# Kernel optimization log

Measured on AMD Instinct MI355X. Metric: run time of the kernel, lower is better.

## Reference

```python
import jax, jax.numpy as jnp
import numpy as np

B, S, HID = 1, 4096, 2048
NH, NKV, D = 16, 4, 128           # num_heads, num_kv_heads, head_dim
QPG = NH // NKV                   # q heads per kv group
GROUP = (QPG + 2) * D             # fused per-group width: Q..Q K V
TOTAL = NKV * GROUP


def setup_inputs() -> dict:
    key = jax.random.key(0)
    k0, k1, k2 = jax.random.split(key, 3)
    x = jax.random.normal(k0, (B, S, HID), dtype=jnp.float32)
    weight_qkv = jax.random.normal(k1, (TOTAL, HID), dtype=jnp.float32) * 0.02
    weight_proj = jax.random.normal(k2, (HID, NH * D), dtype=jnp.float32) * 0.02
    return {"x": x, "weight_qkv": weight_qkv, "weight_proj": weight_proj}


def reference(x, weight_qkv, weight_proj):
    b, s, _ = x.shape
    # fused QKV projection, grouped layout: [b, s, NKV, (QPG+2)*D]
    qkv = jnp.einsum('bsh,ph->bsp', x, weight_qkv).reshape(b, s, NKV, GROUP)
    q = qkv[..., : QPG * D].reshape(b, s, NKV, QPG, D)      # [b,s,g,q,d]
    k = qkv[..., QPG * D:(QPG + 1) * D]                      # [b,s,g,d]
    v = qkv[..., (QPG + 1) * D:]                             # [b,s,g,d]

    scale = 1.0 / jnp.sqrt(jnp.float32(D))
    # GQA causal attention (ring attention at cp_size=1 == full causal attn)
    scores = jnp.einsum('bsgqd,btgd->bgqst', q, k) * scale   # [b,g,q,s,s]
    causal = jnp.tril(jnp.ones((s, s), dtype=bool))
    scores = jnp.where(causal, scores, jnp.finfo(scores.dtype).min)
    attn = jax.nn.softmax(scores, axis=-1)
    out = jnp.einsum('bgqst,btgd->bsgqd', attn, v)           # [b,s,g,q,d]
    out = out.reshape(b, s, NH * D)
    return jnp.einsum('bse,he->bsh', out, weight_proj)       # [b,s,HID]
```

## Files before the change

### kernel.cpp

```cpp
#include <hip/hip_runtime.h>
#include <hip/hip_bf16.h>
#include <stdint.h>

typedef __attribute__((ext_vector_type(8))) short short8;
typedef __attribute__((ext_vector_type(4))) float f32x4;

#define S_LEN   4096
#define HID_DIM 2048
#define NHEAD   16
#define NKV     4
#define DHEAD   128
#define QPG     4
#define GROUP   768
#define TOTAL   3072

#define EXP2F(x) __builtin_amdgcn_exp2f(x)

__device__ __forceinline__ ushort f2bf(float f) {
    union { float f; uint32_t u; } c; c.f = f;
    uint32_t u = c.u;
    u += 0x7fff + ((u >> 16) & 1);
    return (ushort)(u >> 16);
}
__device__ __forceinline__ float bf2f(ushort u) {
    union { uint32_t u; float f; } c; c.u = ((uint32_t)u) << 16;
    return c.f;
}

__device__ __forceinline__ void gld_lds16(const void* g, void* l) {
    __builtin_amdgcn_global_load_lds(
        (const __attribute__((address_space(1))) void*)g,
        (__attribute__((address_space(3))) void*)l, 16, 0, 0);
}

__global__ __launch_bounds__(256)
void cvt_f32_bf16(const float* __restrict__ src, ushort* __restrict__ dst,
                  int n4, int mode)
{
    int i = blockIdx.x * blockDim.x + threadIdx.x;
    int stride = gridDim.x * blockDim.x;
    for (; i < n4; i += stride) {
        float sc = 1.0f;
        if (mode == 1) {
            int row = i >> 9;
            sc = ((row % GROUP) < QPG * DHEAD) ? 0.12751744157413583f : 1.0f;
        }
        float4 v = ((const float4*)src)[i];
        ushort4 o;
        o.x = f2bf(v.x * sc); o.y = f2bf(v.y * sc);
        o.z = f2bf(v.z * sc); o.w = f2bf(v.w * sc);
        ((ushort4*)dst)[i] = o;
    }
}

__device__ __forceinline__ void store_c(ushort* C, size_t idx, float v) { C[idx] = f2bf(v); }
__device__ __forceinline__ void store_c(float*  C, size_t idx, float v) { C[idx] = v; }

template <typename OutT, int NJ, bool WRITE_VT>
__global__ __launch_bounds__(256, 2)
void gemm_bt(const ushort* __restrict__ A, const ushort* __restrict__ B,
             OutT* __restrict__ C, ushort* __restrict__ VT,
             int M, int N, int K)
{
    __shared__ alignas(16) ushort Asl[128 * 32];
    __shared__ alignas(16) ushort Bsl[NJ * 32 * 32];

    const int tid  = threadIdx.x;
    const int wave = tid >> 6;
    const int lane = tid & 63;
    const int quad = lane >> 4;
    const int l15  = lane & 15;
    const int wr   = wave >> 1;
    const int wc   = wave & 1;
    const int m0   = blockIdx.y * 128;
    const int n0   = blockIdx.x * (32 * NJ);

    f32x4 acc[4][NJ];
#pragma unroll
    for (int i = 0; i < 4; i++)
#pragma unroll
        for (int j = 0; j < NJ; j++) acc[i][j] = (f32x4)0.0f;

    for (int kb = 0; kb < K; kb += 32) {
        __syncthreads();
#pragma unroll
        for (int k = 0; k < 2 + NJ / 2; k++) {
            int idx = k * 256 + tid;
            if (idx < 512) {
                const ushort* g = A + (size_t)(m0 + (idx >> 2)) * K + kb + (idx & 3) * 8;
                gld_lds16(g, (char*)Asl + (size_t)(k * 256 + wave * 64) * 16);
            } else {
                int j = idx - 512;
                const ushort* g = B + (size_t)(n0 + (j >> 2)) * K + kb + (j & 3) * 8;
                gld_lds16(g, (char*)Bsl + (size_t)((k - 2) * 256 + wave * 64) * 16);
            }
        }
        __syncthreads();

        short8 af[4], bf[NJ];
#pragma unroll
        for (int i = 0; i < 4; i++)
            af[i] = *(const short8*)(&Asl[(wr * 64 + i * 16 + l15) * 32 + quad * 8]);
#pragma unroll
        for (int j = 0; j < NJ; j++)
            bf[j] = *(const short8*)(&Bsl[(wc * 16 * NJ + j * 16 + l15) * 32 + quad * 8]);
#pragma unroll
        for (int i = 0; i < 4; i++)
#pragma unroll
            for (int j = 0; j < NJ; j++)
                acc[i][j] = __builtin_amdgcn_mfma_f32_16x16x32_bf16(
                    af[i], bf[j], acc[i][j], 0, 0, 0);
    }

#pragma unroll
    for (int j = 0; j < NJ; j++) {
        const int colb = n0 + wc * 16 * NJ + j * 16;
        const int cgrp = colb % GROUP;
        if (WRITE_VT && cgrp >= (QPG + 1) * DHEAD) {
            const int g = colb / GROUP;
            const int d = cgrp - (QPG + 1) * DHEAD + l15;
#pragma unroll
            for (int i = 0; i < 4; i++) {
                int row0 = m0 + wr * 64 + i * 16 + quad * 4;
                ushort4 pk;
                pk.x = f2bf(acc[i][j][0]); pk.y = f2bf(acc[i][j][1]);
                pk.z = f2bf(acc[i][j][2]); pk.w = f2bf(acc[i][j][3]);
                *(ushort4*)(VT + (size_t)(g * 128 + d) * S_LEN + row0) = pk;
            }
        } else {
#pragma unroll
            for (int i = 0; i < 4; i++)
#pragma unroll
                for (int r = 0; r < 4; r++) {
                    int row = m0 + wr * 64 + i * 16 + quad * 4 + r;
                    store_c(C, (size_t)row * N + colb + l15, acc[i][j][r]);
                }
        }
    }
}

__global__ __launch_bounds__(256, 2)
void flash_attn(const ushort* __restrict__ qkv, const ushort* __restrict__ VT,
                ushort* __restrict__ out, ushort* __restrict__ o_part,
                float* __restrict__ l_part)
{
    const int b    = blockIdx.x;
    const int head = b >> 5;
    const int pair = (b >> 1) & 15;
    const int half = b & 1;
    const int g    = head >> 2;
    const int qh   = head & 3;
    const int p_h  = 31 - pair;
    const int H    = 2 * p_h + 2;
    const int hslot = (head * 16 + pair) * 2 + half;

    const int tid  = threadIdx.x;
    const int wave = tid >> 6;
    const int lane = tid & 63;
    const int quad = lane >> 4;
    const int l15  = lane & 15;

    __shared__ alignas(16) ushort Kl[64][136];
    __shared__ alignas(16) ushort Vt[128][72];
    __shared__ alignas(16) ushort Pl[4][32][66];

    int seg_p[2], seg_t0[2], seg_t1[2], seg_part[2];
    int nseg;
    if (half == 0) {
        nseg = 1;
        seg_p[0] = p_h;  seg_t0[0] = 0;  seg_t1[0] = 33;           seg_part[0] = 1;
    } else {
        nseg = 2;
        seg_p[0] = p_h;  seg_t0[0] = 33; seg_t1[0] = H;            seg_part[0] = 1;
        seg_p[1] = pair; seg_t0[1] = 0;  seg_t1[1] = 2 * pair + 2; seg_part[1] = 0;
    }

    const int koff = g * GROUP + QPG * DHEAD;

    for (int s = 0; s < nseg; s++) {
        const int p  = seg_p[s];
        const int t0 = seg_t0[s];
        const int t1 = seg_t1[s];
        const int q0 = p * 128;
        const int base = q0 + wave * 32;

        short8 qf[2][4];
#pragma unroll
        for (int nq = 0; nq < 2; nq++) {
            int row = base + nq * 16 + l15;
            const ushort* qp = qkv + (size_t)row * TOTAL + g * GROUP + qh * DHEAD + quad * 8;
#pragma unroll
            for (int ks = 0; ks < 4; ks++)
                qf[nq][ks] = *(const short8*)(qp + ks * 32);
        }

        f32x4 o[2][8];
#pragma unroll
        for (int oq = 0; oq < 2; oq++)
#pragma unroll
            for (int df = 0; df < 8; df++) o[oq][df] = (f32x4)0.0f;
        float l_vec[2] = {0.0f, 0.0f};

        float4 kpre[4], vpre[4];
#pragma unroll
        for (int r = 0; r < 4; r++) {
            int c = tid + r * 256;
            int kr = c >> 4, kc = c & 15;
            kpre[r] = *(const float4*)(qkv + (size_t)(t0 * 64 + kr) * TOTAL + koff + kc * 8);
            int vd = c >> 3, vc = c & 7;
            vpre[r] = *(const float4*)(VT + (size_t)(g * 128 + vd) * S_LEN + t0 * 64 + vc * 8);
        }

        for (int t = t0; t < t1; t++) {
            __syncthreads();
#pragma unroll
            for (int r = 0; r < 4; r++) {
                int c = tid + r * 256;
                int kr = c >> 4, kc = c & 15;
                *(float4*)(&Kl[kr][kc * 8]) = kpre[r];
                int vd = c >> 3, vc = c & 7;
                *(float4*)(&Vt[vd][vc * 8]) = vpre[r];
            }
            __syncthreads();

            if (t + 1 < t1) {
                const int j1 = (t + 1) * 64;
#pragma unroll
                for (int r = 0; r < 4; r++) {
                    int c = tid + r * 256;
                    int kr = c >> 4, kc = c & 15;
                    kpre[r] = *(const float4*)(qkv + (size_t)(j1 + kr) * TOTAL + koff + kc * 8);
                    int vd = c >> 3, vc = c & 7;
                    vpre[r] = *(const float4*)(VT + (size_t)(g * 128 + vd) * S_LEN + j1 + vc * 8);
                }
            }

            const int j0 = t * 64;
            f32x4 sacc[4][2];
#pragma unroll
            for (int mk = 0; mk < 4; mk++)
#pragma unroll
                for (int nq = 0; nq < 2; nq++) sacc[mk][nq] = (f32x4)0.0f;
#pragma unroll
            for (int mk = 0; mk < 4; mk++)
#pragma unroll
                for (int ks = 0; ks < 4; ks++) {
                    short8 kf = *(const short8*)(&Kl[mk * 16 + l15][ks * 32 + quad * 8]);
#pragma unroll
                    for (int nq = 0; nq < 2; nq++)
                        sacc[mk][nq] = __builtin_amdgcn_mfma_f32_16x16x32_bf16(
                            kf, qf[nq][ks], sacc[mk][nq], 0, 0, 0);
                }

#pragma unroll
            for (int nq = 0; nq < 2; nq++) {
                const int qg = base + nq * 16 + l15;
#pragma unroll
                for (int mk = 0; mk < 4; mk++) {
                    float e0, e1, e2, e3;
                    if (j0 + mk * 16 + 15 > base + nq * 16) {
                        int kv = j0 + mk * 16 + quad * 4;
                        e0 = (kv + 0 > qg) ? 0.0f : EXP2F(sacc[mk][nq][0]);
                        e1 = (kv + 1 > qg) ? 0.0f : EXP2F(sacc[mk][nq][1]);
                        e2 = (kv + 2 > qg) ? 0.0f : EXP2F(sacc[mk][nq][2]);
                        e3 = (kv + 3 > qg) ? 0.0f : EXP2F(sacc[mk][nq][3]);
                    } else {
                        e0 = EXP2F(sacc[mk][nq][0]);
                        e1 = EXP2F(sacc[mk][nq][1]);
                        e2 = EXP2F(sacc[mk][nq][2]);
                        e3 = EXP2F(sacc[mk][nq][3]);
                    }
                    l_vec[nq] += (e0 + e1) + (e2 + e3);
                    ushort4 pk;
                    pk.x = f2bf(e0); pk.y = f2bf(e1);
                    pk.z = f2bf(e2); pk.w = f2bf(e3);
                    *(ushort4*)(&Pl[wave][nq * 16 + l15][mk * 16 + quad * 4]) = pk;
                }
            }

#pragma unroll
            for (int ks = 0; ks < 2; ks++) {
                short8 pf[2];
#pragma unroll
                for (int oq = 0; oq < 2; oq++)
                    pf[oq] = *(const short8*)(&Pl[wave][oq * 16 + l15][ks * 32 + quad * 8]);
#pragma unroll
                for (int df = 0; df < 8; df++) {
                    short8 vf = *(const short8*)(&Vt[df * 16 + l15][ks * 32 + quad * 8]);
#pragma unroll
                    for (int oq = 0; oq < 2; oq++)
                        o[oq][df] = __builtin_amdgcn_mfma_f32_16x16x32_bf16(
                            pf[oq], vf, o[oq][df], 0, 0, 0);
                }
            }
        }

        float l_full[2];
#pragma unroll
        for (int nq = 0; nq < 2; nq++) {
            float l = l_vec[nq];
            l += __shfl_xor(l, 16);
            l += __shfl_xor(l, 32);
            l_full[nq] = l;
        }

        if (seg_part[s]) {
            ushort* po = o_part + (size_t)hslot * 16384;
#pragma unroll
            for (int nq = 0; nq < 2; nq++)
                if (quad == 0)
                    l_part[hslot * 128 + wave * 32 + nq * 16 + l15] = l_full[nq];
#pragma unroll
            for (int oq = 0; oq < 2; oq++)
#pragma unroll
                for (int r = 0; r < 4; r++) {
                    int row_l = wave * 32 + oq * 16 + quad * 4 + r;
#pragma unroll
                    for (int df = 0; df < 8; df++)
                        po[row_l * 128 + df * 16 + l15] = f2bf(o[oq][df][r]);
                }
        } else {
#pragma unroll
            for (int oq = 0; oq < 2; oq++)
#pragma unroll
                for (int r = 0; r < 4; r++) {
                    float lq = __shfl(l_full[oq], quad * 4 + r);
                    float inv = 1.0f / lq;
                    int row = base + oq * 16 + quad * 4 + r;
#pragma unroll
                    for (int df = 0; df < 8; df++) {
                        float v = o[oq][df][r] * inv;
                        out[(size_t)row * (NHEAD * DHEAD) + head * DHEAD
                            + df * 16 + l15] = f2bf(v);
                    }
                }
        }
    }
}

__global__ __launch_bounds__(256)
void fixup_norm(const ushort* __restrict__ o_part, const float* __restrict__ l_part,
                ushort* __restrict__ attn)
{
    const int slot = blockIdx.x;
    const int head = slot >> 4;
    const int pair = slot & 15;
    const int q0   = (31 - pair) * 128;
    const int t    = threadIdx.x;
    const ushort* p0 = o_part + (size_t)(slot * 2) * 16384;
    const ushort* p1 = p0 + 16384;
#pragma unroll 4
    for (int i = 0; i < 64; i++) {
        int idx = i * 256 + t;
        int row = idx >> 7, d = idx & 127;
        float l = l_part[(slot * 2) * 128 + row] + l_part[(slot * 2 + 1) * 128 + row];
        float v = (bf2f(p0[idx]) + bf2f(p1[idx])) / l;
        attn[(size_t)(q0 + row) * HID_DIM + head * DHEAD + d] = f2bf(v);
    }
}

extern "C" void kernel_launch(void* const* d_in, const int* in_sizes, int n_in,
                              void* d_out, int out_size, void* d_ws, size_t ws_size,
                              hipStream_t stream)
{
    const float* x     = (const float*)d_in[0];
    const float* wqkv  = (const float*)d_in[1];
    const float* wproj = (const float*)d_in[2];
    float* outp = (float*)d_out;

    const size_t n_x     = (size_t)S_LEN * HID_DIM;
    const size_t n_wqkv  = (size_t)TOTAL * HID_DIM;
    const size_t n_wproj = (size_t)HID_DIM * HID_DIM;
    const size_t n_qkv   = (size_t)S_LEN * TOTAL;
    const size_t n_attn  = (size_t)S_LEN * HID_DIM;

    ushort* xb     = (ushort*)d_ws;
    ushort* wqkvb  = xb + n_x;
    ushort* qkv    = wqkvb + n_wqkv;
    ushort* attn   = qkv + n_qkv;
    ushort* vt     = attn + n_attn;
    ushort* o_part = xb;
    float*  l_part = (float*)wqkvb;
    ushort* wprojb = wqkvb;

    cvt_f32_bf16<<<2048, 256, 0, stream>>>(x, xb, (int)(n_x / 4), 0);
    cvt_f32_bf16<<<2048, 256, 0, stream>>>(wqkv, wqkvb, (int)(n_wqkv / 4), 1);

    gemm_bt<ushort, 6, true><<<dim3(TOTAL / 192, S_LEN / 128), 256, 0, stream>>>(
        xb, wqkvb, qkv, vt, S_LEN, TOTAL, HID_DIM);

    flash_attn<<<512, 256, 0, stream>>>(qkv, vt, attn, o_part, l_part);
    fixup_norm<<<256, 256, 0, stream>>>(o_part, l_part, attn);

    cvt_f32_bf16<<<2048, 256, 0, stream>>>(wproj, wprojb, (int)(n_wproj / 4), 0);
    gemm_bt<float, 4, false><<<dim3(HID_DIM / 128, S_LEN / 128), 256, 0, stream>>>(
        attn, wprojb, outp, nullptr, S_LEN, HID_DIM, HID_DIM);
}
```

Baseline: 425.3 us.

## Split causal attention work into three equal chunks per query-block pair

Reworks the flash-attention work split from two halves per paired query block to three equal 22-tile chunks over the combined high and low causal rows. This gives 768 blocks with an occupancy hint of 3, which should balance load across CUs and reduce the tail. The fixup kernel now merges up to three partial results per row block and uses ushort4 vectorised loads and stores. The cost is more partial writes and more fixup traffic, plus extra register pressure from the raised launch bound.

```diff
diff --git a/kernel.cpp b/kernel.cpp
--- a/kernel.cpp
+++ b/kernel.cpp
@@ -139,20 +139,21 @@
     }
 }
 
-__global__ __launch_bounds__(256, 2)
+__global__ __launch_bounds__(256, 3)
 void flash_attn(const ushort* __restrict__ qkv, const ushort* __restrict__ VT,
                 ushort* __restrict__ out, ushort* __restrict__ o_part,
                 float* __restrict__ l_part)
 {
     const int b    = blockIdx.x;
-    const int head = b >> 5;
-    const int pair = (b >> 1) & 15;
-    const int half = b & 1;
+    const int head = b / 48;
+    const int rem  = b % 48;
+    const int p    = rem / 3;
+    const int k    = rem % 3;
+    const int pairid = head * 16 + p;
     const int g    = head >> 2;
     const int qh   = head & 3;
-    const int p_h  = 31 - pair;
-    const int H    = 2 * p_h + 2;
-    const int hslot = (head * 16 + pair) * 2 + half;
+    const int T_h  = 64 - 2 * p;
+    const int T_l  = 2 * p + 2;
 
     const int tid  = threadIdx.x;
     const int wave = tid >> 6;
@@ -164,24 +165,33 @@
     __shared__ alignas(16) ushort Vt[128][72];
     __shared__ alignas(16) ushort Pl[4][32][66];
 
-    int seg_p[2], seg_t0[2], seg_t1[2], seg_part[2];
-    int nseg;
-    if (half == 0) {
-        nseg = 1;
-        seg_p[0] = p_h;  seg_t0[0] = 0;  seg_t1[0] = 33;           seg_part[0] = 1;
-    } else {
-        nseg = 2;
-        seg_p[0] = p_h;  seg_t0[0] = 33; seg_t1[0] = H;            seg_part[0] = 1;
-        seg_p[1] = pair; seg_t0[1] = 0;  seg_t1[1] = 2 * pair + 2; seg_part[1] = 0;
+    int sq0[2], st0[2], st1[2], sslot[2], spart[2];
+    int nseg = 0;
+    {
+        const int g0 = 22 * k, g1 = g0 + 22;
+        int a1 = (g1 < T_h) ? g1 : T_h;
+        if (g0 < a1) {
+            sq0[nseg] = 128 * (31 - p); st0[nseg] = g0; st1[nseg] = a1;
+            spart[nseg] = 1; sslot[nseg] = pairid * 3 + k; nseg++;
+        }
+        int b0 = (g0 > T_h) ? g0 : T_h;
+        if (b0 < g1) {
+            int t0l = b0 - T_h, t1l = g1 - T_h;
+            int full = (t0l == 0 && t1l == T_l);
+            sq0[nseg] = 128 * p; st0[nseg] = t0l; st1[nseg] = t1l;
+            spart[nseg] = !full;
+            sslot[nseg] = (k == 1) ? (pairid * 3 + 2)
+                                   : (768 + head * 5 + (p - 11));
+            nseg++;
+        }
     }
 
     const int koff = g * GROUP + QPG * DHEAD;
 
     for (int s = 0; s < nseg; s++) {
-        const int p  = seg_p[s];
-        const int t0 = seg_t0[s];
-        const int t1 = seg_t1[s];
-        const int q0 = p * 128;
+        const int t0 = st0[s];
+        const int t1 = st1[s];
+        const int q0 = sq0[s];
         const int base = q0 + wave * 32;
 
         short8 qf[2][4];
@@ -304,12 +314,13 @@
             l_full[nq] = l;
         }
 
-        if (seg_part[s]) {
-            ushort* po = o_part + (size_t)hslot * 16384;
+        if (spart[s]) {
+            const int slot = sslot[s];
+            ushort* po = o_part + (size_t)slot * 16384;
 #pragma unroll
             for (int nq = 0; nq < 2; nq++)
                 if (quad == 0)
-                    l_part[hslot * 128 + wave * 32 + nq * 16 + l15] = l_full[nq];
+                    l_part[slot * 128 + wave * 32 + nq * 16 + l15] = l_full[nq];
 #pragma unroll
             for (int oq = 0; oq < 2; oq++)
 #pragma unroll
@@ -342,20 +353,40 @@
 void fixup_norm(const ushort* __restrict__ o_part, const float* __restrict__ l_part,
                 ushort* __restrict__ attn)
 {
-    const int slot = blockIdx.x;
-    const int head = slot >> 4;
-    const int pair = slot & 15;
-    const int q0   = (31 - pair) * 128;
-    const int t    = threadIdx.x;
-    const ushort* p0 = o_part + (size_t)(slot * 2) * 16384;
-    const ushort* p1 = p0 + 16384;
-#pragma unroll 4
-    for (int i = 0; i < 64; i++) {
-        int idx = i * 256 + t;
-        int row = idx >> 7, d = idx & 127;
-        float l = l_part[(slot * 2) * 128 + row] + l_part[(slot * 2 + 1) * 128 + row];
-        float v = (bf2f(p0[idx]) + bf2f(p1[idx])) / l;
-        attn[(size_t)(q0 + row) * HID_DIM + head * DHEAD + d] = f2bf(v);
+    const int bid = blockIdx.x;
+    int head, p, q0, ns, sl[3];
+    if (bid < 256) {
+        head = bid >> 4; p = bid & 15;
+        q0 = 128 * (31 - p);
+        ns = (p < 10) ? 3 : 2;
+        int bs = (head * 16 + p) * 3;
+        sl[0] = bs; sl[1] = bs + 1; sl[2] = bs + 2;
+    } else {
+        int idx = bid - 256;
+        head = idx / 5; p = 11 + idx % 5;
+        q0 = 128 * p;
+        ns = 2;
+        sl[0] = (head * 16 + p) * 3 + 2;
+        sl[1] = 768 + head * 5 + (p - 11);
+        sl[2] = 0;
+    }
+    const int t = threadIdx.x;
+#pragma unroll 2
+    for (int i = 0; i < 16; i++) {
+        int e4  = i * 256 + t;
+        int row = e4 >> 5;
+        int d4  = (e4 & 31) * 4;
+        float l = 0.0f, v0 = 0.0f, v1 = 0.0f, v2 = 0.0f, v3 = 0.0f;
+        for (int j = 0; j < ns; j++) {
+            l += l_part[sl[j] * 128 + row];
+            ushort4 u = *(const ushort4*)(o_part + (size_t)sl[j] * 16384 + row * 128 + d4);
+            v0 += bf2f(u.x); v1 += bf2f(u.y); v2 += bf2f(u.z); v3 += bf2f(u.w);
+        }
+        float inv = 1.0f / l;
+        ushort4 w;
+        w.x = f2bf(v0 * inv); w.y = f2bf(v1 * inv);
+        w.z = f2bf(v2 * inv); w.w = f2bf(v3 * inv);
+        *(ushort4*)(attn + (size_t)(q0 + row) * HID_DIM + head * DHEAD + d4) = w;
     }
 }
 
@@ -380,7 +411,7 @@
     ushort* attn   = qkv + n_qkv;
     ushort* vt     = attn + n_attn;
     ushort* o_part = xb;
-    float*  l_part = (float*)wqkvb;
+    float*  l_part = (float*)(o_part + (size_t)848 * 16384);
     ushort* wprojb = wqkvb;
 
     cvt_f32_bf16<<<2048, 256, 0, stream>>>(x, xb, (int)(n_x / 4), 0);
@@ -389,8 +420,8 @@
     gemm_bt<ushort, 6, true><<<dim3(TOTAL / 192, S_LEN / 128), 256, 0, stream>>>(
         xb, wqkvb, qkv, vt, S_LEN, TOTAL, HID_DIM);
 
-    flash_attn<<<512, 256, 0, stream>>>(qkv, vt, attn, o_part, l_part);
-    fixup_norm<<<256, 256, 0, stream>>>(o_part, l_part, attn);
+    flash_attn<<<768, 256, 0, stream>>>(qkv, vt, attn, o_part, l_part);
+    fixup_norm<<<336, 256, 0, stream>>>(o_part, l_part, attn);
 
     cvt_f32_bf16<<<2048, 256, 0, stream>>>(wproj, wprojb, (int)(n_wproj / 4), 0);
     gemm_bt<float, 4, false><<<dim3(HID_DIM / 128, S_LEN / 128), 256, 0, stream>>>(
```

Measured after the change: 539.0 us. +26.7%, slower.
